# Kernel optimization log

Measured on AMD Instinct MI355X. Metric: run time of the kernel, lower is better.

The kernel has to match this reference:

```python
import jax, jax.numpy as jnp
import numpy as np

B, S, T, V, E, H = 32, 64, 64, 32000, 256, 512


def lstm_layer(x, h0, c0, Wih, Whh, bih, bhh):
    """PyTorch-convention LSTM layer. x: [B,T,in]; gates order i,f,g,o."""
    xg = jnp.einsum('bti,gi->btg', x, Wih) + (bih + bhh)  # [B,T,4H] precomputed input gates

    def step(carry, xt):
        h, c = carry
        g = xt + h @ Whh.T
        i, f, gg, o = jnp.split(g, 4, axis=-1)
        c = jax.nn.sigmoid(f) * c + jax.nn.sigmoid(i) * jnp.tanh(gg)
        h = jax.nn.sigmoid(o) * jnp.tanh(c)
        return (h, c), h

    (hT, cT), ys = jax.lax.scan(step, (h0, c0), xg.transpose(1, 0, 2))
    return ys.transpose(1, 0, 2), hT, cT


def setup_inputs() -> dict:
    key = jax.random.key(0)
    ks = jax.random.split(key, 32)
    w = lambda k, shape: jax.random.normal(k, shape, jnp.float32) * 0.05
    return {
        'source': jax.random.randint(ks[0], (B, S), 0, V),
        'target': jax.random.randint(ks[1], (B, T), 0, V),
        'enc_emb': w(ks[2], (V, E)),
        'enc_Wih0': w(ks[3], (4 * H, E)),
        'enc_Whh0': w(ks[4], (4 * H, H)),
        'enc_bih0': w(ks[5], (4 * H,)),
        'enc_bhh0': w(ks[6], (4 * H,)),
        'enc_Wih1': w(ks[7], (4 * H, H)),
        'enc_Whh1': w(ks[8], (4 * H, H)),
        'enc_bih1': w(ks[9], (4 * H,)),
        'enc_bhh1': w(ks[10], (4 * H,)),
        'dec_emb': w(ks[11], (V, E)),
        'dec_Wih0': w(ks[12], (4 * H, E)),
        'dec_Whh0': w(ks[13], (4 * H, H)),
        'dec_bih0': w(ks[14], (4 * H,)),
        'dec_bhh0': w(ks[15], (4 * H,)),
        'dec_Wih1': w(ks[16], (4 * H, H)),
        'dec_Whh1': w(ks[17], (4 * H, H)),
        'dec_bih1': w(ks[18], (4 * H,)),
        'dec_bhh1': w(ks[19], (4 * H,)),
        'aff_W': w(ks[20], (V, H)),
        'aff_b': w(ks[21], (V,)),
    }


def reference(source, target, enc_emb, enc_Wih0, enc_Whh0, enc_bih0, enc_bhh0,
              enc_Wih1, enc_Whh1, enc_bih1, enc_bhh1, dec_emb,
              dec_Wih0, dec_Whh0, dec_bih0, dec_bhh0,
              dec_Wih1, dec_Whh1, dec_bih1, dec_bhh1, aff_W, aff_b):
    b = source.shape[0]
    z = jnp.zeros((b, H), jnp.float32)
    # Encoder: 2-layer LSTM over source, keep final (h,c) per layer
    x = enc_emb[source]                                   # [B,S,E]
    y0, h0, c0 = lstm_layer(x, z, z, enc_Wih0, enc_Whh0, enc_bih0, enc_bhh0)
    _, h1, c1 = lstm_layer(y0, z, z, enc_Wih1, enc_Whh1, enc_bih1, enc_bhh1)
    # Decoder: original loop is always teacher-forced (input = target[:, i]),
    # so it equals one full-sequence LSTM over target[:, :-1].
    dx = dec_emb[target[:, :-1]]                          # [B,T-1,E]
    d0, _, _ = lstm_layer(dx, h0, c0, dec_Wih0, dec_Whh0, dec_bih0, dec_bhh0)
    d1, _, _ = lstm_layer(d0, h1, c1, dec_Wih1, dec_Whh1, dec_bih1, dec_bhh1)
    logits = jnp.einsum('bth,vh->btv', d1, aff_W) + aff_b  # [B,T-1,V]
    # outputs[:,0,:] stays zero as in the original
    return jnp.concatenate([jnp.zeros((b, 1, logits.shape[-1]), logits.dtype), logits], axis=1)
```

## Files before the change

kernel.cpp:

```cpp
#include <hip/hip_runtime.h>
#include <hip/hip_bf16.h>

using bf16 = __hip_bfloat16;
typedef __bf16 bf16x8 __attribute__((ext_vector_type(8)));
typedef float f32x4 __attribute__((ext_vector_type(4)));
typedef int i32x4 __attribute__((ext_vector_type(4)));
typedef short short4v __attribute__((ext_vector_type(4)));
typedef short short8v __attribute__((ext_vector_type(8)));

#define DEV __device__ __forceinline__


DEV unsigned short f2bf(float f) {
  unsigned u = __builtin_bit_cast(unsigned, f);
  u = (u + 0x7fffu + ((u >> 16) & 1u)) >> 16;
  return (unsigned short)u;
}

DEV f32x4 mfma16(bf16x8 a, bf16x8 b, f32x4 c) {
  return __builtin_amdgcn_mfma_f32_16x16x32_bf16(a, b, c, 0, 0, 0);
}

DEV void llc_load16(bf16x8* dst, const bf16* p) {
  i32x4 r;
  asm volatile("global_load_dwordx4 %0, %1, off sc0 sc1" : "=v"(r) : "v"(p) : "memory");
  *dst = __builtin_bit_cast(bf16x8, r);
}
DEV void g_load16(bf16x8* dst, const bf16* p) {
  i32x4 r;
  asm volatile("global_load_dwordx4 %0, %1, off" : "=v"(r) : "v"(p) : "memory");
  *dst = __builtin_bit_cast(bf16x8, r);
}
DEV void llc_store16(void* p, short8v v) {
  asm volatile("global_store_dwordx4 %0, %1, off sc0 sc1"
               :: "v"(p), "v"(__builtin_bit_cast(i32x4, v)) : "memory");
}
DEV void llc_store_f32(float* p, float v) {
  asm volatile("global_store_dword %0, %1, off sc0 sc1" :: "v"(p), "v"(v) : "memory");
}
DEV float llc_load_f32(const float* p) {
  float r;
  asm volatile("global_load_dword %0, %1, off sc0 sc1\n\ts_waitcnt vmcnt(0)"
               : "=v"(r) : "v"(p) : "memory");
  return r;
}
DEV void llc_store_flag(unsigned* p, unsigned v) {
  asm volatile("global_store_dword %0, %1, off sc0 sc1" :: "v"(p), "v"(v) : "memory");
}

DEV void poll16(const unsigned* base, int wave, int lane) {
  const unsigned* p = base + (long)(wave * 16 + (lane & 15)) * 32;
  while (true) {
    unsigned v = __hip_atomic_load(p, __ATOMIC_RELAXED, __HIP_MEMORY_SCOPE_SYSTEM);
    if (__all(v != 0u)) break;
    __builtin_amdgcn_s_sleep(1);
  }
}
DEV void poll64(const unsigned* base, int lane) {
  const unsigned* p = base + (long)lane * 32;
  while (true) {
    unsigned v = __hip_atomic_load(p, __ATOMIC_RELAXED, __HIP_MEMORY_SCOPE_SYSTEM);
    if (__all(v != 0u)) break;
    __builtin_amdgcn_s_sleep(1);
  }
}

struct ConvJobs {
  const float* src[9];
  bf16* dst[9];
  int n[9];
  int cnt;
};

__global__ void convert_all(ConvJobs jobs) {
  long base = (long)blockIdx.x * blockDim.x + threadIdx.x;
  long stride = (long)gridDim.x * blockDim.x;
  for (int ji = 0; ji < jobs.cnt; ++ji) {
    const float* s = jobs.src[ji];
    bf16* d = jobs.dst[ji];
    long n4 = (long)jobs.n[ji] >> 2;
    for (long i = base; i < n4; i += stride) {
      f32x4 v = *(const f32x4*)(s + i * 4);
      short4v o;
#pragma unroll
      for (int j = 0; j < 4; ++j) o[j] = (short)f2bf(v[j]);
      *(short4v*)((short*)d + i * 4) = o;
    }
  }
}

__global__ void embed_gather(const int* __restrict__ ids, const float* __restrict__ emb,
                             bf16* __restrict__ out, int rows, int ids_stride) {
  long total = (long)rows * 64;
  long stride = (long)gridDim.x * blockDim.x;
  for (long i = (long)blockIdx.x * blockDim.x + threadIdx.x; i < total; i += stride) {
    int row = (int)(i >> 6);
    int e = ((int)i & 63) * 4;
    int b = row & 31;
    int t = row >> 5;
    int id = ids[b * ids_stride + t];
    f32x4 v = *(const f32x4*)(emb + (long)id * 256 + e);
    short4v o;
#pragma unroll
    for (int j = 0; j < 4; ++j) o[j] = (short)f2bf(v[j]);
    *(short4v*)((short*)out + (long)row * 256 + e) = o;
  }
}

__global__ void zero_t0(float* __restrict__ out) {
  long total = 32l * 8000;
  long stride = (long)gridDim.x * blockDim.x;
  f32x4 z{};
  for (long i = (long)blockIdx.x * blockDim.x + threadIdx.x; i < total; i += stride) {
    long b = i / 8000;
    long v = i - b * 8000;
    *(f32x4*)(out + b * 64 * 32000 + v * 4) = z;
  }
}

__launch_bounds__(256)
__global__ void gemm_bf16(const bf16* __restrict__ A, const void* __restrict__ Wv, int b_fp32,
                          const float* __restrict__ bias1, const float* __restrict__ bias2,
                          float* __restrict__ C, int M, int N, int K, int affine_remap) {
  __shared__ __align__(16) bf16 As[128][64];
  __shared__ __align__(16) bf16 Bs[128][64];
  int nm = (M + 127) >> 7;
  int mt_blk = blockIdx.x % nm;
  int nt_blk = blockIdx.x / nm;
  long m0 = (long)mt_blk * 128, n0 = (long)nt_blk * 128;
  int tid = threadIdx.x;
  int lane = tid & 63, wave = tid >> 6;
  int wm = wave & 1, wn = wave >> 1;
  int fl = lane & 15, fg = lane >> 4;
  const bf16* Wb = (const bf16*)Wv;
  const float* Wf = (const float*)Wv;
  f32x4 acc[4][4] = {};

  for (int k0 = 0; k0 < K; k0 += 64) {
    __syncthreads();
#pragma unroll
    for (int i = 0; i < 4; ++i) {
      int e = (i * 256 + tid) * 8;
      int row = e >> 6;
      int col = e & 63;
      long ar = m0 + row; if (ar >= M) ar = M - 1;
      *(bf16x8*)(&As[row][col]) = *(const bf16x8*)(A + ar * (long)K + k0 + col);
      long br = n0 + row; if (br >= N) br = N - 1;
      if (b_fp32) {
        const float* p = Wf + br * (long)K + k0 + col;
        f32x4 v0 = *(const f32x4*)p;
        f32x4 v1 = *(const f32x4*)(p + 4);
        short8v o;
#pragma unroll
        for (int j = 0; j < 4; ++j) { o[j] = (short)f2bf(v0[j]); o[j + 4] = (short)f2bf(v1[j]); }
        *(short8v*)(&Bs[row][col]) = o;
      } else {
        *(bf16x8*)(&Bs[row][col]) = *(const bf16x8*)(Wb + br * (long)K + k0 + col);
      }
    }
    __syncthreads();
#pragma unroll
    for (int kt = 0; kt < 2; ++kt) {
      bf16x8 af[4], bfr[4];
#pragma unroll
      for (int x = 0; x < 4; ++x)
        af[x] = *(const bf16x8*)(&As[wm * 64 + x * 16 + fl][kt * 32 + fg * 8]);
#pragma unroll
      for (int x = 0; x < 4; ++x)
        bfr[x] = *(const bf16x8*)(&Bs[wn * 64 + x * 16 + fl][kt * 32 + fg * 8]);
#pragma unroll
      for (int mi = 0; mi < 4; ++mi)
#pragma unroll
        for (int ni = 0; ni < 4; ++ni)
          acc[mi][ni] = mfma16(af[mi], bfr[ni], acc[mi][ni]);
    }
  }
#pragma unroll
  for (int mi = 0; mi < 4; ++mi) {
#pragma unroll
    for (int ni = 0; ni < 4; ++ni) {
#pragma unroll
      for (int r = 0; r < 4; ++r) {
        long row = m0 + wm * 64 + mi * 16 + fg * 4 + r;
        long col = n0 + wn * 64 + ni * 16 + fl;
        if (row < M && col < N) {
          float v = acc[mi][ni][r];
          if (bias1) v += bias1[col];
          if (bias2) v += bias2[col];
          long orow = row;
          if (affine_remap) orow = (long)(row & 31) * 64 + (row >> 5) + 1;
          C[orow * (long)N + col] = v;
        }
      }
    }
  }
}

struct FusedParams {
  const bf16* wih[4]; const bf16* whh[4];
  const float* bih[4]; const float* bhh[4];
  const bf16* x[4];
  bf16* y[4];
  const bf16* hinit[4];
  const float* cinit[4];
  float* cfin[4];
  unsigned* flags;
  const bf16* waff;
  const float* affb;
  float* out;
  unsigned* tile_ctr;
  int do_gemm;
};

DEV unsigned* FL(unsigned* flags, int l, int t) {
  return flags + ((long)(l * 64 + t) * 64) * 32;
}

__launch_bounds__(256)
__global__ void lstm_fused(FusedParams P) {
  __shared__ float part[4][32][33];
  __shared__ __align__(16) unsigned short h_sh[32][8];
  __shared__ __align__(16) bf16 As[128][64];
  __shared__ __align__(16) bf16 Bs[128][64];
  __shared__ unsigned tile_sh;
  const int tid = threadIdx.x;
  const int lane = tid & 63, wave = tid >> 6;
  const int fl = lane & 15, fg = lane >> 4;
  const int l = blockIdx.x >> 6;
  const int slc = blockIdx.x & 63;
  const int n0 = slc * 8;
  const int b_t = tid & 31, d_t = tid >> 5;
  const int T = (l < 2) ? 64 : 63;
  const int Kx = (l & 1) ? 512 : 256;
  const int xspan = Kx >> 2;
  const int ktx = xspan >> 5;
  const bf16* __restrict__ Wih = P.wih[l];
  const bf16* __restrict__ Whh = P.whh[l];
  const bf16* __restrict__ X = P.x[l];
  bf16* __restrict__ Y = P.y[l];
  const bf16* __restrict__ Hinit = P.hinit[l];
  unsigned* flags = P.flags;

  float bsum[4];
#pragma unroll
  for (int gi = 0; gi < 4; ++gi)
    bsum[gi] = P.bih[l][gi * 512 + n0 + d_t] + P.bhh[l][gi * 512 + n0 + d_t];

  bf16x8 wfx[2][4], wfh[2][4];
#pragma unroll
  for (int nt = 0; nt < 2; ++nt) {
    int j = nt * 16 + fl;
    long row = (long)(j >> 3) * 512 + n0 + (j & 7);
#pragma unroll
    for (int kt = 0; kt < 4; ++kt) {
      if (kt < ktx)
        wfx[nt][kt] =
            *(const bf16x8*)(Wih + row * (long)Kx + wave * xspan + kt * 32 + fg * 8);
      wfh[nt][kt] = *(const bf16x8*)(Whh + row * 512l + wave * 128 + kt * 32 + fg * 8);
    }
  }
  float c = 0.f;

  for (int t = 0; t < T; ++t) {
    const unsigned* fb = (l == 1) ? FL(flags, 0, t) : (l == 3) ? FL(flags, 2, t) : nullptr;
    if (fb) poll16(fb, wave, lane);

    const bf16* xb = X + (long)t * 32 * Kx;
    bf16x8 xa0[4], xa1[4];
#pragma unroll
    for (int kt = 0; kt < 4; ++kt) {
      if (kt < ktx) {
        int k = wave * xspan + kt * 32 + fg * 8;
        const bf16* p0 = xb + (long)fl * Kx + k;
        const bf16* p1 = xb + (long)(fl + 16) * Kx + k;
        if (l & 1) {
          llc_load16(&xa0[kt], p0);
          llc_load16(&xa1[kt], p1);
        } else {
          xa0[kt] = *(const bf16x8*)p0;
          xa1[kt] = *(const bf16x8*)p1;
        }
      }
    }
    asm volatile("s_waitcnt vmcnt(0)" ::: "memory");
    __builtin_amdgcn_sched_barrier(0);
    f32x4 acc[2][2] = {};
#pragma unroll
    for (int kt = 0; kt < 4; ++kt) {
      if (kt < ktx) {
        acc[0][0] = mfma16(xa0[kt], wfx[0][kt], acc[0][0]);
        acc[0][1] = mfma16(xa0[kt], wfx[1][kt], acc[0][1]);
        acc[1][0] = mfma16(xa1[kt], wfx[0][kt], acc[1][0]);
        acc[1][1] = mfma16(xa1[kt], wfx[1][kt], acc[1][1]);
      }
    }

    if (t > 0) poll16(FL(flags, l, t - 1), wave, lane);
    else if (l == 2) poll64(FL(flags, 0, 63), lane);
    else if (l == 3) poll64(FL(flags, 1, 63), lane);
    if (t == 0) c = llc_load_f32(P.cinit[l] + (long)b_t * 512 + n0 + d_t);

    const bf16* hb = (t == 0) ? Hinit : (Y + (long)(t - 1) * 32 * 512);
    bf16x8 ha0[4], ha1[4];
#pragma unroll
    for (int kt = 0; kt < 4; ++kt) {
      int k = wave * 128 + kt * 32 + fg * 8;
      llc_load16(&ha0[kt], hb + (long)fl * 512 + k);
      llc_load16(&ha1[kt], hb + (long)(fl + 16) * 512 + k);
    }
    asm volatile("s_waitcnt vmcnt(0)" ::: "memory");
    __builtin_amdgcn_sched_barrier(0);
#pragma unroll
    for (int kt = 0; kt < 4; ++kt) {
      acc[0][0] = mfma16(ha0[kt], wfh[0][kt], acc[0][0]);
      acc[0][1] = mfma16(ha0[kt], wfh[1][kt], acc[0][1]);
      acc[1][0] = mfma16(ha1[kt], wfh[0][kt], acc[1][0]);
      acc[1][1] = mfma16(ha1[kt], wfh[1][kt], acc[1][1]);
    }
#pragma unroll
    for (int mt = 0; mt < 2; ++mt)
#pragma unroll
      for (int nt = 0; nt < 2; ++nt)
#pragma unroll
        for (int r = 0; r < 4; ++r)
          part[wave][mt * 16 + fg * 4 + r][nt * 16 + fl] = acc[mt][nt][r];
    __syncthreads();

    float g4[4];
#pragma unroll
    for (int gi = 0; gi < 4; ++gi) {
      int j = gi * 8 + d_t;
      g4[gi] = part[0][b_t][j] + part[1][b_t][j] + part[2][b_t][j] + part[3][b_t][j] +
               bsum[gi];
    }
    float ig = 1.f / (1.f + __expf(-g4[0]));
    float ff = 1.f / (1.f + __expf(-g4[1]));
    float gg = tanhf(g4[2]);
    float og = 1.f / (1.f + __expf(-g4[3]));
    c = ff * c + ig * gg;
    float h = og * tanhf(c);
    h_sh[b_t][d_t] = f2bf(h);
    if (t == T - 1) {
      llc_store_f32(P.cfin[l] + (long)b_t * 512 + n0 + d_t, c);
      asm volatile("s_waitcnt vmcnt(0)" ::: "memory");
    }
    __syncthreads();
    if (wave == 0) {
      if (lane < 32)
        llc_store16((unsigned short*)Y + ((long)t * 32 + lane) * 512 + n0,
                    *(const short8v*)(&h_sh[lane][0]));
      asm volatile("s_waitcnt vmcnt(0)" ::: "memory");
      if (lane == 0)
        llc_store_flag(FL(flags, l, t) + (long)slc * 32, 1u);
      asm volatile("s_waitcnt vmcnt(0)" ::: "memory");
    }
  }

  if (!P.do_gemm) return;
  const bf16* Ag = P.y[3];
  const bf16* Wg = P.waff;
  const int wm = wave & 1, wn = wave >> 1;
  while (true) {
    if (tid == 0)
      tile_sh = __hip_atomic_fetch_add(P.tile_ctr, 1u, __ATOMIC_RELAXED,
                                       __HIP_MEMORY_SCOPE_AGENT);
    __syncthreads();
    unsigned tile = tile_sh;
    if (tile >= 4000u) break;
    int mt = tile / 250, ntb = tile - mt * 250;
    long m0 = (long)mt * 128, gn0 = (long)ntb * 128;
    if (wave == 0) {
#pragma unroll
      for (int q = 0; q < 4; ++q) {
        int t = mt * 4 + q;
        if (t < 63) {
          const unsigned* f = FL(flags, 3, t) + (long)lane * 32;
          while (__hip_atomic_load(f, __ATOMIC_RELAXED, __HIP_MEMORY_SCOPE_SYSTEM) == 0u)
            __builtin_amdgcn_s_sleep(16);
        }
      }
    }
    __syncthreads();

    f32x4 acc[4][4] = {};
    for (int k0 = 0; k0 < 512; k0 += 64) {
      __syncthreads();
      bf16x8 areg[4], wreg[4];
#pragma unroll
      for (int i = 0; i < 4; ++i) {
        int e = (i * 256 + tid) * 8;
        int row = e >> 6, col = e & 63;
        long ar = m0 + row; if (ar >= 2016) ar = 2015;
        llc_load16(&areg[i], Ag + ar * 512 + k0 + col);
        g_load16(&wreg[i], Wg + (gn0 + row) * 512 + k0 + col);
      }
      asm volatile("s_waitcnt vmcnt(0)" ::: "memory");
#pragma unroll
      for (int i = 0; i < 4; ++i) {
        int e = (i * 256 + tid) * 8;
        int row = e >> 6, col = e & 63;
        *(bf16x8*)(&As[row][col]) = areg[i];
        *(bf16x8*)(&Bs[row][col]) = wreg[i];
      }
      __syncthreads();
#pragma unroll
      for (int kt = 0; kt < 2; ++kt) {
        bf16x8 af[4], bfr[4];
#pragma unroll
        for (int x = 0; x < 4; ++x)
          af[x] = *(const bf16x8*)(&As[wm * 64 + x * 16 + fl][kt * 32 + fg * 8]);
#pragma unroll
        for (int x = 0; x < 4; ++x)
          bfr[x] = *(const bf16x8*)(&Bs[wn * 64 + x * 16 + fl][kt * 32 + fg * 8]);
#pragma unroll
        for (int mi = 0; mi < 4; ++mi)
#pragma unroll
          for (int ni = 0; ni < 4; ++ni)
            acc[mi][ni] = mfma16(af[mi], bfr[ni], acc[mi][ni]);
      }
    }
#pragma unroll
    for (int mi = 0; mi < 4; ++mi) {
#pragma unroll
      for (int ni = 0; ni < 4; ++ni) {
#pragma unroll
        for (int r = 0; r < 4; ++r) {
          long row = m0 + wm * 64 + mi * 16 + fg * 4 + r;
          long col = gn0 + wn * 64 + ni * 16 + fl;
          if (row < 2016) {
            float v = acc[mi][ni][r] + P.affb[col];
            long orow = (long)(row & 31) * 64 + (row >> 5) + 1;
            P.out[orow * 32000 + col] = v;
          }
        }
      }
    }
    __syncthreads();
  }
}

extern "C" void kernel_launch(void* const* d_in, const int* in_sizes, int n_in,
                              void* d_out, int out_size, void* d_ws, size_t ws_size,
                              hipStream_t stream) {
  (void)in_sizes; (void)n_in; (void)out_size;
  const int*   source   = (const int*)d_in[0];
  const int*   target   = (const int*)d_in[1];
  const float* enc_emb  = (const float*)d_in[2];
  const float* enc_Wih0 = (const float*)d_in[3];
  const float* enc_Whh0 = (const float*)d_in[4];
  const float* enc_bih0 = (const float*)d_in[5];
  const float* enc_bhh0 = (const float*)d_in[6];
  const float* enc_Wih1 = (const float*)d_in[7];
  const float* enc_Whh1 = (const float*)d_in[8];
  const float* enc_bih1 = (const float*)d_in[9];
  const float* enc_bhh1 = (const float*)d_in[10];
  const float* dec_emb  = (const float*)d_in[11];
  const float* dec_Wih0 = (const float*)d_in[12];
  const float* dec_Whh0 = (const float*)d_in[13];
  const float* dec_bih0 = (const float*)d_in[14];
  const float* dec_bhh0 = (const float*)d_in[15];
  const float* dec_Wih1 = (const float*)d_in[16];
  const float* dec_Whh1 = (const float*)d_in[17];
  const float* dec_bih1 = (const float*)d_in[18];
  const float* dec_bhh1 = (const float*)d_in[19];
  const float* aff_W    = (const float*)d_in[20];
  const float* aff_b    = (const float*)d_in[21];
  float* out = (float*)d_out;

  size_t off = 0;
  auto alc = [&](size_t bytes) {
    char* p = (char*)d_ws + off;
    off += (bytes + 255) & ~(size_t)255;
    return (void*)p;
  };
  unsigned* FLAGS = (unsigned*)alc((size_t)4 * 64 * 64 * 32 * 4);
  unsigned* TILEC = (unsigned*)alc(256);
  bf16*  ZH  = (bf16*)alc(32 * 512 * 2);
  float* ZC  = (float*)alc(32 * 512 * 4);
  size_t zero_span = off;
  float* CE0 = (float*)alc(32 * 512 * 4);
  float* CE1 = (float*)alc(32 * 512 * 4);
  float* CD  = (float*)alc(32 * 512 * 4);
  float* CD2 = (float*)alc(32 * 512 * 4);
  bf16*  XE  = (bf16*)alc((size_t)2048 * 256 * 2);
  bf16*  XD  = (bf16*)alc((size_t)2016 * 256 * 2);
  bf16*  YE0 = (bf16*)alc((size_t)2048 * 512 * 2);
  bf16*  YE1 = (bf16*)alc((size_t)2048 * 512 * 2);
  bf16*  YD0 = (bf16*)alc((size_t)2016 * 512 * 2);
  bf16*  YD1 = (bf16*)alc((size_t)2016 * 512 * 2);
  bf16*  WI0E = (bf16*)alc((size_t)2048 * 256 * 2);
  bf16*  WH0E = (bf16*)alc((size_t)2048 * 512 * 2);
  bf16*  WI1E = (bf16*)alc((size_t)2048 * 512 * 2);
  bf16*  WH1E = (bf16*)alc((size_t)2048 * 512 * 2);
  bf16*  WI0D = (bf16*)alc((size_t)2048 * 256 * 2);
  bf16*  WH0D = (bf16*)alc((size_t)2048 * 512 * 2);
  bf16*  WI1D = (bf16*)alc((size_t)2048 * 512 * 2);
  bf16*  WH1D = (bf16*)alc((size_t)2048 * 512 * 2);
  bf16*  WAFF = (bf16*)alc((size_t)32000 * 512 * 2);
  bool use_waff = (off <= ws_size);

  hipMemsetAsync(d_ws, 0, zero_span, stream);

  ConvJobs cj;
  cj.src[0] = enc_Wih0; cj.dst[0] = WI0E; cj.n[0] = 2048 * 256;
  cj.src[1] = enc_Whh0; cj.dst[1] = WH0E; cj.n[1] = 2048 * 512;
  cj.src[2] = enc_Wih1; cj.dst[2] = WI1E; cj.n[2] = 2048 * 512;
  cj.src[3] = enc_Whh1; cj.dst[3] = WH1E; cj.n[3] = 2048 * 512;
  cj.src[4] = dec_Wih0; cj.dst[4] = WI0D; cj.n[4] = 2048 * 256;
  cj.src[5] = dec_Whh0; cj.dst[5] = WH0D; cj.n[5] = 2048 * 512;
  cj.src[6] = dec_Wih1; cj.dst[6] = WI1D; cj.n[6] = 2048 * 512;
  cj.src[7] = dec_Whh1; cj.dst[7] = WH1D; cj.n[7] = 2048 * 512;
  cj.cnt = 8;
  if (use_waff) {
    cj.src[8] = aff_W; cj.dst[8] = WAFF; cj.n[8] = 32000 * 512; cj.cnt = 9;
  }
  convert_all<<<dim3(1024), dim3(256), 0, stream>>>(cj);

  embed_gather<<<dim3(512), dim3(256), 0, stream>>>(source, enc_emb, XE, 2048, 64);
  embed_gather<<<dim3(512), dim3(256), 0, stream>>>(target, dec_emb, XD, 2016, 64);
  zero_t0<<<dim3(1000), dim3(256), 0, stream>>>(out);

  FusedParams P;
  P.wih[0] = WI0E; P.whh[0] = WH0E; P.bih[0] = enc_bih0; P.bhh[0] = enc_bhh0;
  P.wih[1] = WI1E; P.whh[1] = WH1E; P.bih[1] = enc_bih1; P.bhh[1] = enc_bhh1;
  P.wih[2] = WI0D; P.whh[2] = WH0D; P.bih[2] = dec_bih0; P.bhh[2] = dec_bhh0;
  P.wih[3] = WI1D; P.whh[3] = WH1D; P.bih[3] = dec_bih1; P.bhh[3] = dec_bhh1;
  P.x[0] = XE;  P.x[1] = YE0; P.x[2] = XD;  P.x[3] = YD0;
  P.y[0] = YE0; P.y[1] = YE1; P.y[2] = YD0; P.y[3] = YD1;
  P.hinit[0] = ZH; P.hinit[1] = ZH;
  P.hinit[2] = YE0 + (size_t)63 * 32 * 512;
  P.hinit[3] = YE1 + (size_t)63 * 32 * 512;
  P.cinit[0] = ZC;  P.cinit[1] = ZC;  P.cinit[2] = CE0; P.cinit[3] = CE1;
  P.cfin[0]  = CE0; P.cfin[1]  = CE1; P.cfin[2]  = CD;  P.cfin[3]  = CD2;
  P.flags = FLAGS;
  P.waff = WAFF; P.affb = aff_b; P.out = out; P.tile_ctr = TILEC;
  P.do_gemm = use_waff ? 1 : 0;
  void* args[1] = {&P};
  hipLaunchCooperativeKernel((void*)lstm_fused, dim3(256), dim3(256), args, 0, stream);

  if (!use_waff)
    gemm_bf16<<<dim3(16 * 250), dim3(256), 0, stream>>>(YD1, aff_W, 1, aff_b, nullptr,
                                                        out, 2016, 32000, 512, 1);
}
```

Measured before the change: 744.3 us.

## Reorder GEMM tiles by vocab column, prefetch next k-slice, swizzle LDS

The output-projection GEMM tail now claims a 128-wide vocab column strip per atomic ticket and walks all 16 row tiles in order. This keeps the W_aff slice hot and follows the decoder's time-step order for flag waits. The k-loop now issues global loads for the next 64-wide slice before the MFMAs on the current one, and LDS tiles use an XOR swizzle to avoid bank conflicts. Output stores go through the LLC store helper. The risk is that a block waits on all later decoder steps inside a single strip, which can serialize the tail when there are few column strips per block.

```diff
diff --git a/kernel.cpp b/kernel.cpp
--- a/kernel.cpp
+++ b/kernel.cpp
@@ -63,6 +63,10 @@
     if (__all(v != 0u)) break;
     __builtin_amdgcn_s_sleep(1);
   }
+}
+
+DEV bf16* swz(bf16* base, int row, int colbyte) {
+  return (bf16*)((char*)base + row * 128 + (colbyte ^ ((row & 7) << 4)));
 }
 
 struct ConvJobs {
@@ -239,7 +243,6 @@
   const bf16* __restrict__ X = P.x[l];
   bf16* __restrict__ Y = P.y[l];
   const bf16* __restrict__ Hinit = P.hinit[l];
-  unsigned* flags = P.flags;
 
   float bsum[4];
 #pragma unroll
@@ -262,7 +265,7 @@
   float c = 0.f;
 
   for (int t = 0; t < T; ++t) {
-    const unsigned* fb = (l == 1) ? FL(flags, 0, t) : (l == 3) ? FL(flags, 2, t) : nullptr;
+    const unsigned* fb = (l == 1) ? FL(P.flags, 0, t) : (l == 3) ? FL(P.flags, 2, t) : nullptr;
     if (fb) poll16(fb, wave, lane);
 
     const bf16* xb = X + (long)t * 32 * Kx;
@@ -295,9 +298,9 @@
       }
     }
 
-    if (t > 0) poll16(FL(flags, l, t - 1), wave, lane);
-    else if (l == 2) poll64(FL(flags, 0, 63), lane);
-    else if (l == 3) poll64(FL(flags, 1, 63), lane);
+    if (t > 0) poll16(FL(P.flags, l, t - 1), wave, lane);
+    else if (l == 2) poll64(FL(P.flags, 0, 63), lane);
+    else if (l == 3) poll64(FL(P.flags, 1, 63), lane);
     if (t == 0) c = llc_load_f32(P.cinit[l] + (long)b_t * 512 + n0 + d_t);
 
     const bf16* hb = (t == 0) ? Hinit : (Y + (long)(t - 1) * 32 * 512);
@@ -351,7 +354,7 @@
                     *(const short8v*)(&h_sh[lane][0]));
       asm volatile("s_waitcnt vmcnt(0)" ::: "memory");
       if (lane == 0)
-        llc_store_flag(FL(flags, l, t) + (long)slc * 32, 1u);
+        llc_store_flag(FL(P.flags, l, t) + (long)slc * 32, 1u);
       asm volatile("s_waitcnt vmcnt(0)" ::: "memory");
     }
   }
@@ -365,77 +368,88 @@
       tile_sh = __hip_atomic_fetch_add(P.tile_ctr, 1u, __ATOMIC_RELAXED,
                                        __HIP_MEMORY_SCOPE_AGENT);
     __syncthreads();
-    unsigned tile = tile_sh;
-    if (tile >= 4000u) break;
-    int mt = tile / 250, ntb = tile - mt * 250;
-    long m0 = (long)mt * 128, gn0 = (long)ntb * 128;
-    if (wave == 0) {
-#pragma unroll
-      for (int q = 0; q < 4; ++q) {
-        int t = mt * 4 + q;
-        if (t < 63) {
-          const unsigned* f = FL(flags, 3, t) + (long)lane * 32;
-          while (__hip_atomic_load(f, __ATOMIC_RELAXED, __HIP_MEMORY_SCOPE_SYSTEM) == 0u)
-            __builtin_amdgcn_s_sleep(16);
+    unsigned s = tile_sh;
+    __syncthreads();
+    if (s >= 250u) break;
+    long gn0 = (long)s * 128;
+
+    for (int mt = 0; mt < 16; ++mt) {
+      if (wave == 0) {
+#pragma unroll
+        for (int q = 0; q < 4; ++q) {
+          int tt = mt * 4 + q;
+          if (tt < 63) {
+            const unsigned* f = FL(P.flags, 3, tt) + (long)lane * 32;
+            while (__hip_atomic_load(f, __ATOMIC_RELAXED, __HIP_MEMORY_SCOPE_SYSTEM) == 0u)
+              __builtin_amdgcn_s_sleep(16);
+          }
         }
       }
-    }
-    __syncthreads();
-
-    f32x4 acc[4][4] = {};
-    for (int k0 = 0; k0 < 512; k0 += 64) {
       __syncthreads();
+
+      long m0 = (long)mt * 128;
+      f32x4 acc[4][4] = {};
       bf16x8 areg[4], wreg[4];
+      int rowv[4], colv[4];
 #pragma unroll
       for (int i = 0; i < 4; ++i) {
         int e = (i * 256 + tid) * 8;
-        int row = e >> 6, col = e & 63;
-        long ar = m0 + row; if (ar >= 2016) ar = 2015;
-        llc_load16(&areg[i], Ag + ar * 512 + k0 + col);
-        g_load16(&wreg[i], Wg + (gn0 + row) * 512 + k0 + col);
-      }
-      asm volatile("s_waitcnt vmcnt(0)" ::: "memory");
-#pragma unroll
-      for (int i = 0; i < 4; ++i) {
-        int e = (i * 256 + tid) * 8;
-        int row = e >> 6, col = e & 63;
-        *(bf16x8*)(&As[row][col]) = areg[i];
-        *(bf16x8*)(&Bs[row][col]) = wreg[i];
-      }
-      __syncthreads();
-#pragma unroll
-      for (int kt = 0; kt < 2; ++kt) {
-        bf16x8 af[4], bfr[4];
-#pragma unroll
-        for (int x = 0; x < 4; ++x)
-          af[x] = *(const bf16x8*)(&As[wm * 64 + x * 16 + fl][kt * 32 + fg * 8]);
-#pragma unroll
-        for (int x = 0; x < 4; ++x)
-          bfr[x] = *(const bf16x8*)(&Bs[wn * 64 + x * 16 + fl][kt * 32 + fg * 8]);
-#pragma unroll
-        for (int mi = 0; mi < 4; ++mi)
-#pragma unroll
-          for (int ni = 0; ni < 4; ++ni)
-            acc[mi][ni] = mfma16(af[mi], bfr[ni], acc[mi][ni]);
-      }
-    }
-#pragma unroll
-    for (int mi = 0; mi < 4; ++mi) {
-#pragma unroll
-      for (int ni = 0; ni < 4; ++ni) {
-#pragma unroll
-        for (int r = 0; r < 4; ++r) {
-          long row = m0 + wm * 64 + mi * 16 + fg * 4 + r;
-          long col = gn0 + wn * 64 + ni * 16 + fl;
-          if (row < 2016) {
-            float v = acc[mi][ni][r] + P.affb[col];
-            long orow = (long)(row & 31) * 64 + (row >> 5) + 1;
-            P.out[orow * 32000 + col] = v;
+        rowv[i] = e >> 6; colv[i] = e & 63;
+        long ar = m0 + rowv[i]; if (ar >= 2016) ar = 2015;
+        llc_load16(&areg[i], Ag + ar * 512 + colv[i]);
+        g_load16(&wreg[i], Wg + (gn0 + rowv[i]) * 512 + colv[i]);
+      }
+      for (int k0 = 0; k0 < 512; k0 += 64) {
+        asm volatile("s_waitcnt vmcnt(0)" ::: "memory");
+        __syncthreads();
+#pragma unroll
+        for (int i = 0; i < 4; ++i) {
+          *(bf16x8*)swz((bf16*)As, rowv[i], colv[i] * 2) = areg[i];
+          *(bf16x8*)swz((bf16*)Bs, rowv[i], colv[i] * 2) = wreg[i];
+        }
+        __syncthreads();
+        if (k0 + 64 < 512) {
+#pragma unroll
+          for (int i = 0; i < 4; ++i) {
+            long ar = m0 + rowv[i]; if (ar >= 2016) ar = 2015;
+            llc_load16(&areg[i], Ag + ar * 512 + (k0 + 64) + colv[i]);
+            g_load16(&wreg[i], Wg + (gn0 + rowv[i]) * 512 + (k0 + 64) + colv[i]);
           }
         }
-      }
-    }
-    __syncthreads();
+#pragma unroll
+        for (int kt = 0; kt < 2; ++kt) {
+          bf16x8 af[4], bfr[4];
+#pragma unroll
+          for (int x = 0; x < 4; ++x)
+            af[x] = *(const bf16x8*)swz((bf16*)As, wm * 64 + x * 16 + fl,
+                                        (kt * 32 + fg * 8) * 2);
+#pragma unroll
+          for (int x = 0; x < 4; ++x)
+            bfr[x] = *(const bf16x8*)swz((bf16*)Bs, wn * 64 + x * 16 + fl,
+                                         (kt * 32 + fg * 8) * 2);
+#pragma unroll
+          for (int mi = 0; mi < 4; ++mi)
+#pragma unroll
+            for (int ni = 0; ni < 4; ++ni)
+              acc[mi][ni] = mfma16(af[mi], bfr[ni], acc[mi][ni]);
+        }
+      }
+#pragma unroll
+      for (int mi = 0; mi < 4; ++mi)
+#pragma unroll
+        for (int ni = 0; ni < 4; ++ni)
+#pragma unroll
+          for (int r = 0; r < 4; ++r) {
+            long row = m0 + wm * 64 + mi * 16 + fg * 4 + r;
+            long col = gn0 + wn * 64 + ni * 16 + fl;
+            if (row < 2016) {
+              float v = acc[mi][ni][r] + P.affb[col];
+              long orow = (long)(row & 31) * 64 + (row >> 5) + 1;
+              llc_store_f32(P.out + orow * 32000 + col, v);
+            }
+          }
+      __syncthreads();
+    }
   }
 }
 
```

New measurement: 974.0 us. +30.9%, slower.
